# Kernel optimization log

Measured on AMD Instinct MI355X. Metric: run time of the kernel, lower is better.

## Reference

```python
import jax, jax.numpy as jnp
import numpy as np

THETA = 10000.0
NUM_HEADS = 16


def _rope_tables(seq_len, d_k, dtype):
    exponent = jnp.arange(d_k // 2, dtype=jnp.float32) * (2.0 / d_k)
    inv_freq = THETA ** (-exponent)                      # (d_k/2,)
    pos = jnp.arange(seq_len, dtype=jnp.float32)
    angles = pos[:, None] * inv_freq[None, :]            # (n, d_k/2)
    return jnp.cos(angles).astype(dtype), jnp.sin(angles).astype(dtype)


def _apply_rope(x, cos, sin):
    # x: (..., n, d_k); interleaved pair convention: pairs are (x[...,2i], x[...,2i+1])
    x1 = x[..., 0::2]
    x2 = x[..., 1::2]
    r1 = x1 * cos - x2 * sin
    r2 = x1 * sin + x2 * cos
    return jnp.stack([r1, r2], axis=-1).reshape(x.shape)


def setup_inputs() -> dict:
    key = jax.random.key(0)
    ks = jax.random.split(key, 5)
    B, N, D = 2, 4096, 1024
    std = (2.0 / (D + D)) ** 0.5
    return {
        "x": jax.random.normal(ks[0], (B, N, D), dtype=jnp.float32),
        "Wq": jax.random.normal(ks[1], (D, D), dtype=jnp.float32) * std,
        "Wk": jax.random.normal(ks[2], (D, D), dtype=jnp.float32) * std,
        "Wv": jax.random.normal(ks[3], (D, D), dtype=jnp.float32) * std,
        "Wo": jax.random.normal(ks[4], (D, D), dtype=jnp.float32) * std,
    }


def reference(x, Wq, Wk, Wv, Wo):
    B, N, D = x.shape
    H = NUM_HEADS
    d_k = D // H

    def proj(W):
        y = jnp.einsum('oi,bni->bno', W, x)
        return y.reshape(B, N, H, d_k).transpose(0, 2, 1, 3)  # (b,h,n,d)

    Q, K, V = proj(Wq), proj(Wk), proj(Wv)

    cos, sin = _rope_tables(N, d_k, x.dtype)
    Q = _apply_rope(Q, cos, sin)
    K = _apply_rope(K, cos, sin)

    scores = jnp.einsum('bhnd,bhmd->bhnm', Q, K) / jnp.sqrt(jnp.asarray(d_k, x.dtype))
    causal = jnp.tril(jnp.ones((N, N), dtype=bool))
    scores = jnp.where(causal, scores, -jnp.inf)
    attn = jax.nn.softmax(scores, axis=-1)
    out = jnp.einsum('bhnm,bhmd->bhnd', attn, V)          # (b,h,n,d)
    out = out.transpose(0, 2, 1, 3).reshape(B, N, D)
    return jnp.einsum('oi,bni->bno', Wo, out)
```

## Files before the change

### kernel.cpp

```cpp
#include <hip/hip_runtime.h>
#include <hip/hip_bf16.h>
#include <stdint.h>

typedef __attribute__((ext_vector_type(8))) short short8;
typedef __attribute__((ext_vector_type(4))) float f32x4;
typedef __attribute__((ext_vector_type(2))) unsigned uint32x2;

#define NSEQ 4096
#define DMODEL 1024
#define MROWS 8192

__device__ __forceinline__ unsigned short f2bf(float f) {
  union { float f; unsigned u; } v; v.f = f;
  unsigned r = v.u + 0x7fffu + ((v.u >> 16) & 1u);
  return (unsigned short)(r >> 16);
}

__device__ __forceinline__ unsigned pkc(float lo, float hi) {
  unsigned r;
  asm("v_cvt_pk_bf16_f32 %0, %1, %2" : "=v"(r) : "v"(lo), "v"(hi));
  return r;
}

__device__ __forceinline__ void gload16(const unsigned short* g, unsigned short* l) {
  __builtin_amdgcn_global_load_lds(
      (const __attribute__((address_space(1))) unsigned int*)g,
      (__attribute__((address_space(3))) unsigned int*)l, 16, 0, 0);
}

__device__ __forceinline__ void pexch(unsigned x, unsigned y, unsigned& w_lo, unsigned& w_hi) {
  uint32x2 t = __builtin_amdgcn_permlane32_swap(x, y, false, false);
  uint32x2 u = __builtin_amdgcn_permlane16_swap(t[0], t[1], false, false);
  w_lo = u[0];
  w_hi = u[1];
}

__global__ void k_conv(const float* __restrict__ src, unsigned short* __restrict__ dst) {
  int i = (blockIdx.x * 256 + threadIdx.x) * 4;
  float4 v = *(const float4*)(src + i);
  ushort4 o;
  o.x = f2bf(v.x); o.y = f2bf(v.y); o.z = f2bf(v.z); o.w = f2bf(v.w);
  *(ushort4*)(dst + i) = o;
}

__global__ void k_convw(const float* __restrict__ s0, const float* __restrict__ s1,
                        const float* __restrict__ s2, const float* __restrict__ s3,
                        unsigned short* __restrict__ dst) {
  int z = blockIdx.x >> 10;
  const float* src = (z == 0) ? s0 : (z == 1) ? s1 : (z == 2) ? s2 : s3;
  float sc = (z == 0) ? 0.18033688011112042f : 1.0f;
  int i = ((blockIdx.x & 1023) * 256 + threadIdx.x) * 4;
  float4 v = *(const float4*)(src + i);
  ushort4 o;
  o.x = f2bf(v.x * sc); o.y = f2bf(v.y * sc); o.z = f2bf(v.z * sc); o.w = f2bf(v.w * sc);
  *(ushort4*)(dst + (size_t)z * 1048576 + i) = o;
}

__global__ void k_rope_tab(float* __restrict__ cosT, float* __restrict__ sinT) {
  int i = blockIdx.x * 256 + threadIdx.x;
  int pos = i >> 5, j = i & 31;
  float invf = exp2f(-(float)j * 0.41524101186092029f);
  float ang = (float)pos * invf;
  cosT[i] = cosf(ang);
  sinT[i] = sinf(ang);
}

__global__ __launch_bounds__(256) void k_gemm_bt(
    const unsigned short* __restrict__ A,
    const unsigned short* __restrict__ Bw,
    unsigned short* __restrict__ obf,
    unsigned short* __restrict__ Vt,
    float* __restrict__ of32,
    const float* __restrict__ cosT, const float* __restrict__ sinT,
    int K, int modeArg) {
  const int N = DMODEL;
  const int q8 = gridDim.x >> 3;
  const int wg = (blockIdx.x & 7) * q8 + (blockIdx.x >> 3);
  const int z = wg >> 9;
  const int rr = wg & 511;
  const int bn = rr & 7, bm = rr >> 3;
  const int mode = (modeArg < 0) ? z : modeArg;
  const unsigned short* Bz = Bw + (size_t)z * DMODEL * K;
  unsigned short* oz = (obf && mode <= 1) ? (obf + (size_t)z * MROWS * DMODEL) : nullptr;

  const int t = threadIdx.x;
  const int w = t >> 6, lane = t & 63;
  const int wr = w >> 1, wc = w & 1;
  const int lr = lane & 15, lg = lane >> 4;

  __shared__ __align__(16) unsigned short SM[2][128 * 64];
  unsigned short* Al = SM[0];
  unsigned short* Bl = SM[1];

  const unsigned short* Ab = A + (size_t)bm * 128 * K;
  const unsigned short* Bb = Bz + (size_t)bn * 128 * K;
  const int trow = t >> 3, tcol = (t & 7) * 8;

  f32x4 acc[4][4] = {};

  for (int k0 = 0; k0 < K; k0 += 64) {
#pragma unroll
    for (int c = 0; c < 4; ++c) {
      gload16(Ab + (size_t)(c * 32 + trow) * K + k0 + tcol, &Al[c * 2048 + t * 8]);
      gload16(Bb + (size_t)(c * 32 + trow) * K + k0 + tcol, &Bl[c * 2048 + t * 8]);
    }
    asm volatile("s_waitcnt vmcnt(0)" ::: "memory");
    __syncthreads();
#pragma unroll
    for (int kk = 0; kk < 2; ++kk) {
      short8 af[4], bfr[4];
#pragma unroll
      for (int mi = 0; mi < 4; ++mi)
        af[mi] = *(const short8*)&Al[(wr * 64 + mi * 16 + lr) * 64 + kk * 32 + lg * 8];
#pragma unroll
      for (int ni = 0; ni < 4; ++ni)
        bfr[ni] = *(const short8*)&Bl[(wc * 64 + ni * 16 + lr) * 64 + kk * 32 + lg * 8];
#pragma unroll
      for (int mi = 0; mi < 4; ++mi)
#pragma unroll
        for (int ni = 0; ni < 4; ++ni)
          acc[mi][ni] = __builtin_amdgcn_mfma_f32_16x16x32_bf16(af[mi], bfr[ni], acc[mi][ni], 0, 0, 0);
    }
    __syncthreads();
  }

  if (mode <= 1 || mode == 3) {
    float* Cf = (float*)&SM[0][0];
#pragma unroll
    for (int half = 0; half < 2; ++half) {
      if (half) __syncthreads();
      if (wr == half) {
#pragma unroll
        for (int mi = 0; mi < 4; ++mi)
#pragma unroll
          for (int ni = 0; ni < 4; ++ni)
#pragma unroll
            for (int r = 0; r < 4; ++r) {
              int row = mi * 16 + lg * 4 + r;
              int col = (wc * 64 + ni * 16 + lr) ^ (lg << 3);
              Cf[row * 128 + col] = acc[mi][ni][r];
            }
      }
      __syncthreads();
      int pr = t >> 2;
      int gm = bm * 128 + half * 64 + pr;
      int xorv = ((pr >> 2) & 3) << 3;
      if (mode == 3) {
        float* orow = of32 + (size_t)gm * N + bn * 128;
#pragma unroll
        for (int k = 0; k < 4; ++k) {
          int c0 = (t & 3) * 8 + k * 32;
          int cs = c0 ^ xorv;
          float4 va = *(const float4*)&Cf[pr * 128 + cs];
          float4 vb = *(const float4*)&Cf[pr * 128 + cs + 4];
          *(float4*)(orow + c0) = va;
          *(float4*)(orow + c0 + 4) = vb;
        }
      } else {
        int pos = gm & (NSEQ - 1);
        const float* cB = cosT + pos * 32;
        const float* sB = sinT + pos * 32;
        unsigned short* orow = oz + (size_t)gm * N + bn * 128;
#pragma unroll
        for (int k = 0; k < 4; ++k) {
          int c0 = (t & 3) * 8 + k * 32;
          int cs = c0 ^ xorv;
          float4 va = *(const float4*)&Cf[pr * 128 + cs];
          float4 vb = *(const float4*)&Cf[pr * 128 + cs + 4];
          int j0 = (c0 & 63) >> 1;
          float4 cv = *(const float4*)&cB[j0];
          float4 sv = *(const float4*)&sB[j0];
          uint4 o;
          o.x = pkc(va.x * cv.x - va.y * sv.x, va.x * sv.x + va.y * cv.x);
          o.y = pkc(va.z * cv.y - va.w * sv.y, va.z * sv.y + va.w * cv.y);
          o.z = pkc(vb.x * cv.z - vb.y * sv.z, vb.x * sv.z + vb.y * cv.z);
          o.w = pkc(vb.z * cv.w - vb.w * sv.w, vb.z * sv.w + vb.w * cv.w);
          *(uint4*)(orow + c0) = o;
        }
      }
    }
  } else {
#pragma unroll
    for (int mi = 0; mi < 4; ++mi)
#pragma unroll
      for (int ni = 0; ni < 4; ++ni) {
        int gm0 = bm * 128 + wr * 64 + mi * 16 + lg * 4;
        int gn = bn * 128 + wc * 64 + ni * 16 + lr;
        int b = gm0 >> 12, n = gm0 & (NSEQ - 1);
        int h = gn >> 6, d = gn & 63;
        uint2 u;
        u.x = pkc(acc[mi][ni][0], acc[mi][ni][1]);
        u.y = pkc(acc[mi][ni][2], acc[mi][ni][3]);
        *(uint2*)(Vt + ((size_t)((b * 16 + h) * 64 + d)) * NSEQ + n) = u;
      }
  }
}

__global__ __launch_bounds__(256, 2) void k_attn12(
    const unsigned short* __restrict__ Qb,
    const unsigned short* __restrict__ Kb,
    const unsigned short* __restrict__ Vtg,
    unsigned short* __restrict__ AO) {
  const int id = blockIdx.x;
  const int bh = id & 31;
  const int pq = id >> 5;
  const int b = bh >> 4, h = bh & 15;
  const int t = threadIdx.x;
  const int w = t >> 6, lane = t & 63;
  const int lr = lane & 15, hi4 = lane >> 4;
  const size_t rowbase = (size_t)b * NSEQ;

  __shared__ __align__(16) unsigned short Kl[2][64 * 64];
  __shared__ __align__(16) unsigned short Vl[2][64 * 64];
  __shared__ __align__(16) unsigned short Pl[4][16 * 64];

  const int pswz = (lr & 7) << 3;

  short8 ones;
#pragma unroll
  for (int i = 0; i < 8; ++i) ones[i] = (short)0x3F80;

#define STAGE(buf, kv0)                                                                   \
  {                                                                                       \
    _Pragma("unroll")                                                                     \
    for (int it = 0; it < 2; ++it) {                                                      \
      int c = t + it * 256;                                                               \
      int row = c >> 3, sg = (c & 7) ^ (row & 7);                                         \
      gload16(Kb + (rowbase + (kv0) + row) * DMODEL + h * 64 + sg * 8, &Kl[buf][c * 8]);  \
      gload16(Vtg + ((size_t)bh * 64 + row) * NSEQ + (kv0) + sg * 8, &Vl[buf][c * 8]);    \
    }                                                                                     \
  }

#pragma unroll
  for (int qi = 0; qi < 2; ++qi) {
    const int qt = qi ? pq : (31 - pq);
    const int q0w = qt * 128 + w * 32;

    short8 qf[2][2];
#pragma unroll
    for (int sub = 0; sub < 2; ++sub) {
      const unsigned short* qp = Qb + (rowbase + q0w + sub * 16 + lr) * DMODEL + h * 64 + hi4 * 8;
#pragma unroll
      for (int s = 0; s < 2; ++s)
        qf[sub][s] = *(const short8*)(qp + s * 32);
    }

    f32x4 oacc[2][4] = {};
    f32x4 lacc[2] = {};
    const int nkv = (qt + 1) * 2;

    STAGE(0, 0);
    asm volatile("s_waitcnt vmcnt(0)" ::: "memory");
    __syncthreads();

    for (int ib = 0; ib < nkv; ++ib) {
      const int kv0 = ib * 64, cur = ib & 1;
      if (ib + 1 < nkv) STAGE(cur ^ 1, kv0 + 64);

      if (kv0 <= q0w + 31) {
        short8 Kf[4][2], Vf[2][4];
#pragma unroll
        for (int t4 = 0; t4 < 4; ++t4)
#pragma unroll
          for (int s = 0; s < 2; ++s)
            Kf[t4][s] = *(const short8*)&Kl[cur][(t4 * 16 + lr) * 64 + (((s * 4 + hi4) ^ (lr & 7)) * 8)];
#pragma unroll
        for (int c = 0; c < 2; ++c)
#pragma unroll
          for (int dt = 0; dt < 4; ++dt)
            Vf[c][dt] = *(const short8*)&Vl[cur][(dt * 16 + lr) * 64 + (((c * 4 + hi4) ^ (lr & 7)) * 8)];

#pragma unroll
        for (int sub = 0; sub < 2; ++sub) {
          const int qs = q0w + sub * 16;
          const int qlane = qs + lr;
          f32x4 sa[4];
          const f32x4 zz = {0.f, 0.f, 0.f, 0.f};
          __builtin_amdgcn_s_setprio(1);
#pragma unroll
          for (int t4 = 0; t4 < 4; ++t4) {
            f32x4 x = __builtin_amdgcn_mfma_f32_16x16x32_bf16(Kf[t4][0], qf[sub][0], zz, 0, 0, 0);
            sa[t4] = __builtin_amdgcn_mfma_f32_16x16x32_bf16(Kf[t4][1], qf[sub][1], x, 0, 0, 0);
          }
          __builtin_amdgcn_s_setprio(0);
          if (kv0 + 63 > qs) {
#pragma unroll
            for (int t4 = 0; t4 < 4; ++t4)
#pragma unroll
              for (int r = 0; r < 4; ++r)
                if (kv0 + t4 * 16 + hi4 * 4 + r > qlane) sa[t4][r] = -1e30f;
          }
#pragma unroll
          for (int t4 = 0; t4 < 4; ++t4)
#pragma unroll
            for (int r = 0; r < 4; ++r)
              sa[t4][r] = __builtin_amdgcn_exp2f(sa[t4][r]);

          unsigned a0 = pkc(sa[0][0], sa[0][1]), a1 = pkc(sa[0][2], sa[0][3]);
          unsigned a2 = pkc(sa[1][0], sa[1][1]), a3 = pkc(sa[1][2], sa[1][3]);
          unsigned a4 = pkc(sa[2][0], sa[2][1]), a5 = pkc(sa[2][2], sa[2][3]);
          unsigned a6 = pkc(sa[3][0], sa[3][1]), a7 = pkc(sa[3][2], sa[3][3]);
          unsigned w0, w1, w2, w3, x0, x1, x2, x3;
          pexch(a0, a2, w0, w2);
          pexch(a1, a3, w1, w3);
          pexch(a4, a6, x0, x2);
          pexch(a5, a7, x1, x3);
          union { uint4 u; short8 s; } P0, P1;
          P0.u.x = w0; P0.u.y = w1; P0.u.z = w2; P0.u.w = w3;
          P1.u.x = x0; P1.u.y = x1; P1.u.z = x2; P1.u.w = x3;
          short8 pf0 = P0.s;
          short8 pf1 = P1.s;

          __builtin_amdgcn_s_setprio(1);
#pragma unroll
          for (int dt = 0; dt < 4; ++dt) {
            oacc[sub][dt] = __builtin_amdgcn_mfma_f32_16x16x32_bf16(Vf[0][dt], pf0, oacc[sub][dt], 0, 0, 0);
            oacc[sub][dt] = __builtin_amdgcn_mfma_f32_16x16x32_bf16(Vf[1][dt], pf1, oacc[sub][dt], 0, 0, 0);
          }
          lacc[sub] = __builtin_amdgcn_mfma_f32_16x16x32_bf16(ones, pf0, lacc[sub], 0, 0, 0);
          lacc[sub] = __builtin_amdgcn_mfma_f32_16x16x32_bf16(ones, pf1, lacc[sub], 0, 0, 0);
          __builtin_amdgcn_s_setprio(0);
        }
      }
      asm volatile("s_waitcnt vmcnt(0)" ::: "memory");
      __syncthreads();
    }

#pragma unroll
    for (int sub = 0; sub < 2; ++sub) {
      float inv = 1.f / lacc[sub][0];
#pragma unroll
      for (int dt = 0; dt < 4; ++dt) {
        uint2 u;
        u.x = pkc(oacc[sub][dt][0] * inv, oacc[sub][dt][1] * inv);
        u.y = pkc(oacc[sub][dt][2] * inv, oacc[sub][dt][3] * inv);
        *(uint2*)&Pl[w][lr * 64 + ((dt * 16 + hi4 * 4) ^ pswz)] = u;
      }
      asm volatile("s_waitcnt lgkmcnt(0)" ::: "memory");
      __builtin_amdgcn_sched_barrier(0);
      int q2 = lane >> 2, ch = (lane & 3) * 16;
      int qswz = (q2 & 7) << 3;
      uint4 r0 = *(const uint4*)&Pl[w][q2 * 64 + (ch ^ qswz)];
      uint4 r1 = *(const uint4*)&Pl[w][q2 * 64 + ((ch + 8) ^ qswz)];
      unsigned short* op = AO + (rowbase + q0w + sub * 16 + q2) * DMODEL + h * 64 + ch;
      *(uint4*)op = r0;
      *(uint4*)(op + 8) = r1;
      __syncthreads();
    }
  }
}

extern "C" void kernel_launch(void* const* d_in, const int* in_sizes, int n_in,
                              void* d_out, int out_size, void* d_ws, size_t ws_size,
                              hipStream_t stream) {
  const float* x  = (const float*)d_in[0];
  const float* Wq = (const float*)d_in[1];
  const float* Wk = (const float*)d_in[2];
  const float* Wv = (const float*)d_in[3];
  const float* Wo = (const float*)d_in[4];
  float* out = (float*)d_out;
  char* ws = (char*)d_ws;

  unsigned short* xb  = (unsigned short*)(ws);
  unsigned short* Wb  = (unsigned short*)(ws + 16777216);
  unsigned short* Qb  = (unsigned short*)(ws + 25165824);
  unsigned short* Kb  = Qb + 8388608;
  unsigned short* Vtg = (unsigned short*)(ws + 58720256);
  unsigned short* AO  = (unsigned short*)(ws + 75497472);
  float* cosT = (float*)(ws + 92274688);
  float* sinT = (float*)(ws + 92798976);

  k_conv<<<8192, 256, 0, stream>>>(x, xb);
  k_convw<<<4096, 256, 0, stream>>>(Wq, Wk, Wv, Wo, Wb);
  k_rope_tab<<<512, 256, 0, stream>>>(cosT, sinT);

  k_gemm_bt<<<1536, 256, 0, stream>>>(xb, Wb, Qb, Vtg, nullptr, cosT, sinT, DMODEL, -1);

  k_attn12<<<512, 256, 0, stream>>>(Qb, Kb, Vtg, AO);

  k_gemm_bt<<<512, 256, 0, stream>>>(AO, Wb + 3145728, nullptr, nullptr, out, cosT, sinT, DMODEL, 3);
}
```

Measured before the change: 219.7 us.

## Triple-buffer K/V tiles in attention with partial vmcnt waits

Moves the attention kernel's K/V shared-memory staging from double to triple buffering, prefetching two tiles ahead. Each iteration waits only for the oldest tile with vmcnt(8) instead of draining all loads. Fragments are read into registers before a barrier so the freed buffer can be refilled while MFMA work runs. LDS use grows by a third, which may lower occupancy, and the extra prefetches at the tail are clamped to the last tile, so some loads are redundant.

```diff
diff --git a/kernel.cpp b/kernel.cpp
--- a/kernel.cpp
+++ b/kernel.cpp
@@ -196,7 +196,7 @@
   }
 }
 
-__global__ __launch_bounds__(256, 2) void k_attn12(
+__global__ __launch_bounds__(256, 2) void k_attn14(
     const unsigned short* __restrict__ Qb,
     const unsigned short* __restrict__ Kb,
     const unsigned short* __restrict__ Vtg,
@@ -210,8 +210,8 @@
   const int lr = lane & 15, hi4 = lane >> 4;
   const size_t rowbase = (size_t)b * NSEQ;
 
-  __shared__ __align__(16) unsigned short Kl[2][64 * 64];
-  __shared__ __align__(16) unsigned short Vl[2][64 * 64];
+  __shared__ __align__(16) unsigned short Kl[3][64 * 64];
+  __shared__ __align__(16) unsigned short Vl[3][64 * 64];
   __shared__ __align__(16) unsigned short Pl[4][16 * 64];
 
   const int pswz = (lr & 7) << 3;
@@ -248,17 +248,21 @@
     f32x4 oacc[2][4] = {};
     f32x4 lacc[2] = {};
     const int nkv = (qt + 1) * 2;
+    const int kvlast = (nkv - 1) * 64;
 
     STAGE(0, 0);
-    asm volatile("s_waitcnt vmcnt(0)" ::: "memory");
-    __syncthreads();
-
+    STAGE(1, (64 < kvlast ? 64 : kvlast));
+    STAGE(2, (128 < kvlast ? 128 : kvlast));
+    asm volatile("s_waitcnt vmcnt(8)" ::: "memory");
+    __builtin_amdgcn_s_barrier();
+
+    int cur = 0;
     for (int ib = 0; ib < nkv; ++ib) {
-      const int kv0 = ib * 64, cur = ib & 1;
-      if (ib + 1 < nkv) STAGE(cur ^ 1, kv0 + 64);
-
-      if (kv0 <= q0w + 31) {
-        short8 Kf[4][2], Vf[2][4];
+      const int kv0 = ib * 64;
+      const bool live = (kv0 <= q0w + 31);
+
+      short8 Kf[4][2], Vf[2][4];
+      if (live) {
 #pragma unroll
         for (int t4 = 0; t4 < 4; ++t4)
 #pragma unroll
@@ -269,7 +273,18 @@
 #pragma unroll
           for (int dt = 0; dt < 4; ++dt)
             Vf[c][dt] = *(const short8*)&Vl[cur][(dt * 16 + lr) * 64 + (((c * 4 + hi4) ^ (lr & 7)) * 8)];
-
+        asm volatile("s_waitcnt lgkmcnt(0)" ::: "memory");
+        __builtin_amdgcn_sched_barrier(0);
+      }
+      __builtin_amdgcn_s_barrier();
+
+      {
+        int kvn = kv0 + 192;
+        if (kvn > kvlast) kvn = kvlast;
+        STAGE(cur, kvn);
+      }
+
+      if (live) {
 #pragma unroll
         for (int sub = 0; sub < 2; ++sub) {
           const int qs = q0w + sub * 16;
@@ -322,9 +337,14 @@
           __builtin_amdgcn_s_setprio(0);
         }
       }
-      asm volatile("s_waitcnt vmcnt(0)" ::: "memory");
-      __syncthreads();
-    }
+
+      asm volatile("s_waitcnt vmcnt(8)" ::: "memory");
+      __builtin_amdgcn_s_barrier();
+      cur = (cur == 2) ? 0 : cur + 1;
+    }
+
+    asm volatile("s_waitcnt vmcnt(0)" ::: "memory");
+    __builtin_amdgcn_s_barrier();
 
 #pragma unroll
     for (int sub = 0; sub < 2; ++sub) {
@@ -345,7 +365,8 @@
       unsigned short* op = AO + (rowbase + q0w + sub * 16 + q2) * DMODEL + h * 64 + ch;
       *(uint4*)op = r0;
       *(uint4*)(op + 8) = r1;
-      __syncthreads();
+      asm volatile("s_waitcnt lgkmcnt(0)" ::: "memory");
+      __builtin_amdgcn_sched_barrier(0);
     }
   }
 }
@@ -376,7 +397,7 @@
 
   k_gemm_bt<<<1536, 256, 0, stream>>>(xb, Wb, Qb, Vtg, nullptr, cosT, sinT, DMODEL, -1);
 
-  k_attn12<<<512, 256, 0, stream>>>(Qb, Kb, Vtg, AO);
+  k_attn14<<<512, 256, 0, stream>>>(Qb, Kb, Vtg, AO);
 
   k_gemm_bt<<<512, 256, 0, stream>>>(AO, Wb + 3145728, nullptr, nullptr, out, cosT, sinT, DMODEL, 3);
 }
```

Result: no change. 220.0 us (+0.1%).
